# Kernel tuning notes

Hardware: AMD Instinct MI355X
Metric: run time of the kernel (lower is better)

Reference implementation:

```python
import jax, jax.numpy as jnp
import numpy as np
import math

L, B = 1024, 256
SEQ_DIM, KMER_DIM, HID = 16, 256, 64
N_LAYERS = 2
IN_DIM = SEQ_DIM + KMER_DIM + 21  # 293


def _normalize(v, eps=1e-12):
    return v / jnp.maximum(jnp.linalg.norm(v, axis=-1, keepdims=True), eps)


def _nerf_rot(a, b, c):
    # rotation matrix with columns [bc, n x bc, n] from last three backbone points
    bc = _normalize(c - b)
    n = _normalize(jnp.cross(b - a, bc))
    return jnp.stack([bc, jnp.cross(n, bc), n], axis=-1)  # (..., 3, 3)


def pnerf(c_tilde, nfrag):
    # c_tilde: (3L, B, 3) SRF coordinates; parallelized natural extension of reference frame
    Ltot, batch = c_tilde.shape[0], c_tilde.shape[1]
    k = Ltot // nfrag
    # contiguous fragments of length k, folded into the batch dim: (k, nfrag*B, 3)
    x = c_tilde.reshape(nfrag, k, batch, 3).transpose(1, 0, 2, 3).reshape(k, nfrag * batch, 3)
    init = jnp.array([[-math.sqrt(0.5), math.sqrt(1.5), 0.0],
                      [-math.sqrt(2.0), 0.0, 0.0],
                      [0.0, 0.0, 0.0]], dtype=c_tilde.dtype)
    F = nfrag * batch
    carry0 = (jnp.broadcast_to(init[0], (F, 3)),
              jnp.broadcast_to(init[1], (F, 3)),
              jnp.broadcast_to(init[2], (F, 3)))

    def extend(carry, ct):
        a, b, c = carry
        R = _nerf_rot(a, b, c)                      # (F, 3, 3)
        d = c + jnp.einsum('fij,fj->fi', R, ct)     # (F, 3)
        return (b, c, d), d

    _, frag = jax.lax.scan(extend, carry0, x)        # (k, F, 3)
    frag = frag.reshape(k, nfrag, batch, 3).transpose(1, 0, 2, 3)  # (nfrag, k, B, 3)

    # assemble fragments sequentially; init frame is identity/origin so frag 0 passes through
    carryA = (jnp.broadcast_to(init[0], (batch, 3)),
              jnp.broadcast_to(init[1], (batch, 3)),
              jnp.broadcast_to(init[2], (batch, 3)))

    def assemble(carry, fr):
        a, b, c = carry
        R = _nerf_rot(a, b, c)                      # (B, 3, 3)
        y = c + jnp.einsum('bij,kbj->kbi', R, fr)   # (k, B, 3)
        return (y[-3], y[-2], y[-1]), y

    _, ys = jax.lax.scan(assemble, carryA, frag)     # (nfrag, k, B, 3)
    return ys.reshape(nfrag * k, batch, 3)


def setup_inputs() -> dict:
    key = jax.random.key(0)
    ks = jax.random.split(key, 12)
    s = 0.05
    return {
        'seq': jax.random.randint(ks[0], (L, B), 0, 20, dtype=jnp.int64),
        'kmer': jax.random.randint(ks[1], (L, B), 0, 22 ** 3, dtype=jnp.int64),
        'pssm': jax.random.uniform(ks[2], (L, B, 21), dtype=jnp.float32),
        'length': jax.random.randint(ks[3], (L,), 1, L, dtype=jnp.int64),
        'seq_embed': jax.random.normal(ks[4], (20, SEQ_DIM), dtype=jnp.float32) * s,
        'kmer_embed': jax.random.normal(ks[5], (22 ** 3, KMER_DIM), dtype=jnp.float32) * s,
        'W0': jax.random.normal(ks[6], (IN_DIM, HID), dtype=jnp.float32) * s,
        'b0': jnp.zeros((HID,), dtype=jnp.float32),
        'We': jax.random.normal(ks[7], (HID, HID), dtype=jnp.float32) * s,
        'be': jnp.zeros((HID,), dtype=jnp.float32),
        'W1': jax.random.normal(ks[8], (HID, 9), dtype=jnp.float32) * s,
        'b1': jnp.zeros((9,), dtype=jnp.float32),
    }


def reference(seq, kmer, pssm, length, seq_embed, kmer_embed, W0, b0, We, be, W1, b1):
    s = seq_embed[seq]                                   # (L, B, 16)
    km = kmer_embed[kmer]                                # (L, B, 256)
    h = jnp.concatenate([s, km, pssm], axis=2)           # (L, B, 293)
    h = h @ W0 + b0                                      # (L, B, 64)
    # torch list-multiplication shares the SAME Linear across the n_layers blocks
    for _ in range(N_LAYERS):
        h = jax.nn.relu(h @ We + be)                     # dropout is identity at eval
    srf = h @ W1 + b1                                    # (L, B, 9)
    Ld, Bd = srf.shape[0], srf.shape[1]
    srf = srf.reshape(Ld, Bd, 3, 3).transpose(0, 2, 1, 3).reshape(3 * Ld, Bd, 3)
    return pnerf(srf, int(math.sqrt(Ld)))
```

## Files before the change

kernel.cpp:

```cpp
#include <hip/hip_runtime.h>
#include <math.h>

#define HPAD 72
#define PPAD 40

typedef short bf16x8 __attribute__((ext_vector_type(8)));
typedef float f32x4  __attribute__((ext_vector_type(4)));

__device__ __forceinline__ unsigned short f2bf(float x) {
    unsigned int u = __float_as_uint(x);
    return (unsigned short)((u + 0x7FFFu + ((u >> 16) & 1u)) >> 16);
}
__device__ __forceinline__ float bf2f(unsigned short h) {
    return __uint_as_float(((unsigned int)h) << 16);
}
__device__ __forceinline__ void split2(float x, unsigned short& h, unsigned short& l) {
    h = f2bf(x);
    l = f2bf(x - bf2f(h));
}
__device__ __forceinline__ void split2t(float x, unsigned short& h, unsigned short& l) {
    unsigned int u = __float_as_uint(x);
    h = (unsigned short)(u >> 16);
    float r = x - __uint_as_float(u & 0xFFFF0000u);
    l = f2bf(r);
}

__device__ __forceinline__ float inv_norm3(float x, float y, float z) {
    float d = fmaf(x, x, fmaf(y, y, z * z));
    return rsqrtf(fmaxf(d, 1e-24f));
}
__device__ __forceinline__ float3 f3sub(float3 a, float3 b) {
    return make_float3(a.x - b.x, a.y - b.y, a.z - b.z);
}
__device__ __forceinline__ float3 f3cross(float3 a, float3 b) {
    return make_float3(a.y * b.z - a.z * b.y,
                       a.z * b.x - a.x * b.z,
                       a.x * b.y - a.y * b.x);
}
__device__ __forceinline__ void nerf_frame(const float3& A, const float3& Bv,
                                           const float3& C, float3& bc,
                                           float3& n, float3& m3) {
    float3 w  = f3sub(C, Bv);
    float3 v  = f3sub(Bv, A);
    float3 cr = f3cross(v, w);
    float iw = inv_norm3(w.x, w.y, w.z);
    float ic = inv_norm3(cr.x, cr.y, cr.z);
    bc = make_float3(w.x * iw, w.y * iw, w.z * iw);
    n  = make_float3(cr.x * ic, cr.y * ic, cr.z * ic);
    m3 = f3cross(n, bc);
}
__device__ __forceinline__ float3 nerf_place(const float3& C, const float3& bc,
                                             const float3& m3, const float3& n,
                                             float tx, float ty, float tz) {
    return make_float3(
        fmaf(m3.x, ty, fmaf(bc.x, tx, fmaf(n.x, tz, C.x))),
        fmaf(m3.y, ty, fmaf(bc.y, tx, fmaf(n.y, tz, C.y))),
        fmaf(m3.z, ty, fmaf(bc.z, tx, fmaf(n.z, tz, C.z))));
}

__global__ __launch_bounds__(256) void tables_kernel(
    const float* __restrict__ emb, const float* __restrict__ W0,
    const float* __restrict__ se, const float* __restrict__ b0,
    const float* __restrict__ We, const float* __restrict__ W1,
    float* __restrict__ kt, float* __restrict__ seqT,
    unsigned short* __restrict__ WeTH, unsigned short* __restrict__ WeTL,
    unsigned short* __restrict__ W0pTH, unsigned short* __restrict__ W0pTL,
    unsigned short* __restrict__ W1TH, unsigned short* __restrict__ W1TL) {
    __shared__ float W0s[256][64];
    int tid = threadIdx.x;
    if (blockIdx.x < 333) {
        for (int i = tid; i < 16384; i += 256)
            W0s[i >> 6][i & 63] = W0[16 * 64 + i];
        __syncthreads();
        int j  = tid & 63;
        int wv = tid >> 6;
        int r0 = blockIdx.x * 32 + wv * 8;
        float acc[8] = {0.f,0.f,0.f,0.f,0.f,0.f,0.f,0.f};
        #pragma unroll 8
        for (int k = 0; k < 256; ++k) {
            float w = W0s[k][j];
            #pragma unroll
            for (int r = 0; r < 8; ++r) {
                int rr = r0 + r; if (rr > 10647) rr = 10647;
                acc[r] = fmaf(emb[rr * 256 + k], w, acc[r]);
            }
        }
        #pragma unroll
        for (int r = 0; r < 8; ++r)
            if (r0 + r < 10648) kt[(r0 + r) * 64 + j] = acc[r];
    } else if (blockIdx.x < 338) {
        int e = (blockIdx.x - 333) * 256 + tid;
        int r = e >> 6, j = e & 63;
        float acc = b0[j];
        #pragma unroll
        for (int k = 0; k < 16; ++k)
            acc = fmaf(se[r * 16 + k], W0[k * 64 + j], acc);
        float cs = 0.f;
        #pragma unroll
        for (int c = 0; c < 21; ++c) cs += W0[(272 + c) * 64 + j];
        seqT[r * 64 + j] = acc + 0.5f * cs;
    } else {
        #pragma unroll
        for (int i = 0; i < 16; ++i) {
            int e = i * 256 + tid;
            int k = e >> 6, n = e & 63;
            unsigned short h, l; split2(We[k * 64 + n], h, l);
            WeTH[n * 64 + k] = h; WeTL[n * 64 + k] = l;
        }
        #pragma unroll
        for (int i = 0; i < 8; ++i) {
            int e = i * 256 + tid;
            int k = e >> 6, n = e & 63;
            float w = (k < 21) ? W0[(272 + k) * 64 + n] : 0.f;
            unsigned short h, l; split2(w, h, l);
            W0pTH[n * 32 + k] = h; W0pTL[n * 32 + k] = l;
        }
        #pragma unroll
        for (int i = 0; i < 4; ++i) {
            int e = i * 256 + tid;
            int k = e >> 4, c = e & 15;
            float w = (c < 9) ? W1[k * 9 + c] : 0.f;
            unsigned short h, l; split2(w, h, l);
            W1TH[c * 64 + k] = h; W1TL[c * 64 + k] = l;
        }
    }
}

__global__ __launch_bounds__(256, 4) void mlp_kernel(
    const int* __restrict__ seq, const int* __restrict__ kmer,
    const float* __restrict__ pssm,
    const float* __restrict__ seqT, const float* __restrict__ kmerT,
    const unsigned short* __restrict__ WeTH, const unsigned short* __restrict__ WeTL,
    const unsigned short* __restrict__ W0pTH, const unsigned short* __restrict__ W0pTL,
    const unsigned short* __restrict__ W1TH, const unsigned short* __restrict__ W1TL,
    const float* __restrict__ be, const float* __restrict__ b1,
    float* __restrict__ srf_t) {

    __shared__ __align__(16) unsigned short Hah[64][HPAD];
    __shared__ __align__(16) unsigned short Hal[64][HPAD];
    __shared__ __align__(16) unsigned short ovl[2][64][HPAD];
    __shared__ int sidx[64];
    __shared__ int kidx[64];

    unsigned short (*Ph)[PPAD] = (unsigned short(*)[PPAD])(&ovl[0][0][0]);
    unsigned short (*Pl)[PPAD] = (unsigned short(*)[PPAD])(&ovl[0][0][0] + 2560);
    unsigned short (*Hbh)[HPAD] = ovl[0];
    unsigned short (*Hbl)[HPAD] = ovl[1];

    const int tid  = threadIdx.x;
    const int lane = tid & 63;
    const int wv   = __builtin_amdgcn_readfirstlane(tid >> 6);
    const int q    = lane >> 4;
    const int c16  = lane & 15;
    const int m0   = blockIdx.x * 64;
    const int n    = wv * 16 + c16;

    if (tid < 64) {
        sidx[tid] = seq[m0 + tid];
        kidx[tid] = kmer[m0 + tid];
    }
    for (int i = tid; i < 64 * 21; i += 256) {
        float v = pssm[m0 * 21 + i] - 0.5f;
        unsigned short h, l; split2t(v, h, l);
        Ph[i / 21][i % 21] = h;
        Pl[i / 21][i % 21] = l;
    }
    for (int i = tid; i < 64 * 11; i += 256) {
        Ph[i / 11][21 + (i % 11)] = 0;
        Pl[i / 11][21 + (i % 11)] = 0;
    }

    bf16x8 WeH[2], WeL[2], W1H[2], W1L[2], W0H, W0L;
    #pragma unroll
    for (int kk = 0; kk < 2; ++kk) {
        WeH[kk] = *(const bf16x8*)(WeTH + n * 64 + kk * 32 + q * 8);
        WeL[kk] = *(const bf16x8*)(WeTL + n * 64 + kk * 32 + q * 8);
        W1H[kk] = *(const bf16x8*)(W1TH + c16 * 64 + kk * 32 + q * 8);
        W1L[kk] = *(const bf16x8*)(W1TL + c16 * 64 + kk * 32 + q * 8);
    }
    W0H = *(const bf16x8*)(W0pTH + n * 32 + q * 8);
    W0L = *(const bf16x8*)(W0pTL + n * 32 + q * 8);
    const float be_n = be[n];
    const float b1h  = (c16 < 9) ? b1[c16] : 0.f;
    __syncthreads();

    f32x4 acc[4];
    #pragma unroll
    for (int t = 0; t < 4; ++t) {
        #pragma unroll
        for (int r = 0; r < 4; ++r) {
            int m = t * 16 + q * 4 + r;
            acc[t][r] = seqT[sidx[m] * 64 + n] + kmerT[kidx[m] * 64 + n];
        }
    }
    #pragma unroll
    for (int t = 0; t < 4; ++t) {
        bf16x8 ah = *(const bf16x8*)&Ph[t * 16 + c16][q * 8];
        bf16x8 al = *(const bf16x8*)&Pl[t * 16 + c16][q * 8];
        acc[t] = __builtin_amdgcn_mfma_f32_16x16x32_bf16(ah, W0H, acc[t], 0, 0, 0);
        acc[t] = __builtin_amdgcn_mfma_f32_16x16x32_bf16(al, W0H, acc[t], 0, 0, 0);
        acc[t] = __builtin_amdgcn_mfma_f32_16x16x32_bf16(ah, W0L, acc[t], 0, 0, 0);
    }
    #pragma unroll
    for (int t = 0; t < 4; ++t)
        #pragma unroll
        for (int r = 0; r < 4; ++r) {
            unsigned short h, l; split2t(acc[t][r], h, l);
            Hah[t * 16 + q * 4 + r][n] = h;
            Hal[t * 16 + q * 4 + r][n] = l;
        }
    __syncthreads();

    {
        f32x4 a1[4];
        #pragma unroll
        for (int t = 0; t < 4; ++t) {
            a1[t] = (f32x4){be_n, be_n, be_n, be_n};
            #pragma unroll
            for (int kk = 0; kk < 2; ++kk) {
                bf16x8 ah = *(const bf16x8*)&Hah[t * 16 + c16][kk * 32 + q * 8];
                bf16x8 al = *(const bf16x8*)&Hal[t * 16 + c16][kk * 32 + q * 8];
                a1[t] = __builtin_amdgcn_mfma_f32_16x16x32_bf16(ah, WeH[kk], a1[t], 0, 0, 0);
                a1[t] = __builtin_amdgcn_mfma_f32_16x16x32_bf16(al, WeH[kk], a1[t], 0, 0, 0);
                a1[t] = __builtin_amdgcn_mfma_f32_16x16x32_bf16(ah, WeL[kk], a1[t], 0, 0, 0);
            }
        }
        #pragma unroll
        for (int t = 0; t < 4; ++t)
            #pragma unroll
            for (int r = 0; r < 4; ++r) {
                unsigned short h, l; split2t(fmaxf(a1[t][r], 0.f), h, l);
                Hbh[t * 16 + q * 4 + r][n] = h;
                Hbl[t * 16 + q * 4 + r][n] = l;
            }
        __syncthreads();
    }
    {
        f32x4 a2[4];
        #pragma unroll
        for (int t = 0; t < 4; ++t) {
            a2[t] = (f32x4){be_n, be_n, be_n, be_n};
            #pragma unroll
            for (int kk = 0; kk < 2; ++kk) {
                bf16x8 ah = *(const bf16x8*)&Hbh[t * 16 + c16][kk * 32 + q * 8];
                bf16x8 al = *(const bf16x8*)&Hbl[t * 16 + c16][kk * 32 + q * 8];
                a2[t] = __builtin_amdgcn_mfma_f32_16x16x32_bf16(ah, WeH[kk], a2[t], 0, 0, 0);
                a2[t] = __builtin_amdgcn_mfma_f32_16x16x32_bf16(al, WeH[kk], a2[t], 0, 0, 0);
                a2[t] = __builtin_amdgcn_mfma_f32_16x16x32_bf16(ah, WeL[kk], a2[t], 0, 0, 0);
            }
        }
        #pragma unroll
        for (int t = 0; t < 4; ++t)
            #pragma unroll
            for (int r = 0; r < 4; ++r) {
                unsigned short h, l; split2t(fmaxf(a2[t][r], 0.f), h, l);
                Hah[t * 16 + q * 4 + r][n] = h;
                Hal[t * 16 + q * 4 + r][n] = l;
            }
        __syncthreads();
    }

    {
        f32x4 ah4 = (f32x4){b1h, b1h, b1h, b1h};
        #pragma unroll
        for (int kk = 0; kk < 2; ++kk) {
            bf16x8 ah = *(const bf16x8*)&Hah[wv * 16 + c16][kk * 32 + q * 8];
            bf16x8 al = *(const bf16x8*)&Hal[wv * 16 + c16][kk * 32 + q * 8];
            ah4 = __builtin_amdgcn_mfma_f32_16x16x32_bf16(ah, W1H[kk], ah4, 0, 0, 0);
            ah4 = __builtin_amdgcn_mfma_f32_16x16x32_bf16(al, W1H[kk], ah4, 0, 0, 0);
            ah4 = __builtin_amdgcn_mfma_f32_16x16x32_bf16(ah, W1L[kk], ah4, 0, 0, 0);
        }
        if (c16 < 9) {
            #pragma unroll
            for (int r = 0; r < 4; ++r) {
                int pos = m0 + wv * 16 + q * 4 + r;
                int l = pos >> 8, b = pos & 255;
                srf_t[(l * 9 + c16) * 256 + b] = ah4[r];
            }
        }
    }
}

__global__ __launch_bounds__(64) void extend_kernel(
    const float* __restrict__ srf_t, float* __restrict__ fragbuf,
    float* __restrict__ FPbuf) {
    int frag = blockIdx.x >> 2;
    int bb   = ((blockIdx.x & 3) << 6) + threadIdx.x;

    float3 A  = make_float3(-0.70710678118654752f, 1.22474487139158905f, 0.f);
    float3 Bv = make_float3(-1.41421356237309505f, 0.f, 0.f);
    float3 C  = make_float3(0.f, 0.f, 0.f);

    float ct0[9], ct1[9], ct2[9];
    #pragma unroll
    for (int m = 0; m < 9; ++m) {
        ct0[m] = srf_t[((frag * 32 + 0) * 9 + m) * 256 + bb];
        ct1[m] = srf_t[((frag * 32 + 1) * 9 + m) * 256 + bb];
    }

    for (int ll = 0; ll < 32; ++ll) {
        if (ll < 30) {
            #pragma unroll
            for (int m = 0; m < 9; ++m)
                ct2[m] = srf_t[((frag * 32 + ll + 2) * 9 + m) * 256 + bb];
        } else {
            #pragma unroll
            for (int m = 0; m < 9; ++m) ct2[m] = 0.f;
        }
        #pragma unroll
        for (int s3 = 0; s3 < 3; ++s3) {
            float3 bc, nn, m3;
            nerf_frame(A, Bv, C, bc, nn, m3);
            float3 d = nerf_place(C, bc, m3, nn,
                                  ct0[3 * s3 + 0], ct0[3 * s3 + 1], ct0[3 * s3 + 2]);
            int row = frag * 96 + ll * 3 + s3;
            fragbuf[(row * 3 + 0) * 256 + bb] = d.x;
            fragbuf[(row * 3 + 1) * 256 + bb] = d.y;
            fragbuf[(row * 3 + 2) * 256 + bb] = d.z;
            A = Bv; Bv = C; C = d;
        }
        #pragma unroll
        for (int m = 0; m < 9; ++m) { ct0[m] = ct1[m]; ct1[m] = ct2[m]; }
    }

    float3 bc, nn, m3;
    nerf_frame(A, Bv, C, bc, nn, m3);
    FPbuf[(frag * 12 + 0)  * 256 + bb] = bc.x;
    FPbuf[(frag * 12 + 1)  * 256 + bb] = bc.y;
    FPbuf[(frag * 12 + 2)  * 256 + bb] = bc.z;
    FPbuf[(frag * 12 + 3)  * 256 + bb] = m3.x;
    FPbuf[(frag * 12 + 4)  * 256 + bb] = m3.y;
    FPbuf[(frag * 12 + 5)  * 256 + bb] = m3.z;
    FPbuf[(frag * 12 + 6)  * 256 + bb] = nn.x;
    FPbuf[(frag * 12 + 7)  * 256 + bb] = nn.y;
    FPbuf[(frag * 12 + 8)  * 256 + bb] = nn.z;
    FPbuf[(frag * 12 + 9)  * 256 + bb] = C.x;
    FPbuf[(frag * 12 + 10) * 256 + bb] = C.y;
    FPbuf[(frag * 12 + 11) * 256 + bb] = C.z;
}

__global__ __launch_bounds__(256) void carry_kernel(
    const float* __restrict__ FPbuf, float4* __restrict__ frames) {
    __shared__ float S[384][64];
    int tid  = threadIdx.x;
    int base = blockIdx.x * 64;
    for (int i = tid; i < 384 * 64; i += 256) {
        int row = i >> 6, col = i & 63;
        S[row][col] = FPbuf[row * 256 + base + col];
    }
    __syncthreads();
    if (tid < 64) {
        int bb = base + tid;
        float3 ob = make_float3(1.f, 0.f, 0.f);
        float3 om = make_float3(0.f, 1.f, 0.f);
        float3 on = make_float3(0.f, 0.f, 1.f);
        float3 c  = make_float3(0.f, 0.f, 0.f);
        for (int f = 0; f < 32; ++f) {
            int fb = (f * 256 + bb) * 3;
            frames[fb + 0] = make_float4(ob.x, ob.y, ob.z, om.x);
            frames[fb + 1] = make_float4(om.y, om.z, on.x, on.y);
            frames[fb + 2] = make_float4(on.z, c.x, c.y, c.z);

            int r0 = f * 12;
            float3 Fb = make_float3(S[r0+0][tid], S[r0+1][tid], S[r0+2][tid]);
            float3 Fm = make_float3(S[r0+3][tid], S[r0+4][tid], S[r0+5][tid]);
            float3 Fn = make_float3(S[r0+6][tid], S[r0+7][tid], S[r0+8][tid]);
            float3 p  = make_float3(S[r0+9][tid], S[r0+10][tid], S[r0+11][tid]);

            float3 nb = make_float3(
                fmaf(ob.x,Fb.x, fmaf(om.x,Fb.y, on.x*Fb.z)),
                fmaf(ob.y,Fb.x, fmaf(om.y,Fb.y, on.y*Fb.z)),
                fmaf(ob.z,Fb.x, fmaf(om.z,Fb.y, on.z*Fb.z)));
            float3 nm = make_float3(
                fmaf(ob.x,Fm.x, fmaf(om.x,Fm.y, on.x*Fm.z)),
                fmaf(ob.y,Fm.x, fmaf(om.y,Fm.y, on.y*Fm.z)),
                fmaf(ob.z,Fm.x, fmaf(om.z,Fm.y, on.z*Fm.z)));
            float3 nn = make_float3(
                fmaf(ob.x,Fn.x, fmaf(om.x,Fn.y, on.x*Fn.z)),
                fmaf(ob.y,Fn.x, fmaf(om.y,Fn.y, on.y*Fn.z)),
                fmaf(ob.z,Fn.x, fmaf(om.z,Fn.y, on.z*Fn.z)));
            float3 nc = make_float3(
                fmaf(ob.x,p.x, fmaf(om.x,p.y, fmaf(on.x,p.z, c.x))),
                fmaf(ob.y,p.x, fmaf(om.y,p.y, fmaf(on.y,p.z, c.y))),
                fmaf(ob.z,p.x, fmaf(om.z,p.y, fmaf(on.z,p.z, c.z))));
            ob = nb; om = nm; on = nn; c = nc;
        }
    }
}

__global__ __launch_bounds__(256) void apply_kernel(
    const float* __restrict__ fragbuf, const float4* __restrict__ frames,
    float* __restrict__ out) {
    __shared__ float sm[768];
    int bb   = threadIdx.x;
    int row  = blockIdx.x;
    int frag = row / 96;

    float fx = fragbuf[(row * 3 + 0) * 256 + bb];
    float fy = fragbuf[(row * 3 + 1) * 256 + bb];
    float fz = fragbuf[(row * 3 + 2) * 256 + bb];

    int fb = (frag * 256 + bb) * 3;
    float4 f0 = frames[fb + 0];
    float4 f1 = frames[fb + 1];
    float4 f2 = frames[fb + 2];

    sm[bb * 3 + 0] = f2.y + f0.x * fx + f0.w * fy + f1.z * fz;
    sm[bb * 3 + 1] = f2.z + f0.y * fx + f1.x * fy + f1.w * fz;
    sm[bb * 3 + 2] = f2.w + f0.z * fx + f1.y * fy + f2.x * fz;
    __syncthreads();

    int base = row * 768;
    out[base + bb]       = sm[bb];
    out[base + 256 + bb] = sm[256 + bb];
    out[base + 512 + bb] = sm[512 + bb];
}

extern "C" void kernel_launch(void* const* d_in, const int* in_sizes, int n_in,
                              void* d_out, int out_size, void* d_ws, size_t ws_size,
                              hipStream_t stream) {
    const int*   seq        = (const int*)d_in[0];
    const int*   kmer       = (const int*)d_in[1];
    const float* pssm       = (const float*)d_in[2];
    const float* seq_embed  = (const float*)d_in[4];
    const float* kmer_embed = (const float*)d_in[5];
    const float* W0         = (const float*)d_in[6];
    const float* b0         = (const float*)d_in[7];
    const float* We         = (const float*)d_in[8];
    const float* be         = (const float*)d_in[9];
    const float* W1         = (const float*)d_in[10];
    const float* b1         = (const float*)d_in[11];

    float* ws      = (float*)d_ws;
    float* kmerT   = ws;
    float* seqT    = kmerT + 681472;
    float* srf_t   = seqT + 1280;
    float* fragbuf = srf_t + 2359296;
    float* frames  = fragbuf + 2359296;
    float* FPbuf   = frames + 98304;
    float* out     = (float*)d_out;

    unsigned short* WeTH  = (unsigned short*)fragbuf;
    unsigned short* WeTL  = WeTH + 4096;
    unsigned short* W0pTH = WeTL + 4096;
    unsigned short* W0pTL = W0pTH + 2048;
    unsigned short* W1TH  = W0pTL + 2048;
    unsigned short* W1TL  = W1TH + 1024;

    hipLaunchKernelGGL(tables_kernel, dim3(339), dim3(256), 0, stream,
                       kmer_embed, W0, seq_embed, b0, We, W1,
                       kmerT, seqT, WeTH, WeTL, W0pTH, W0pTL, W1TH, W1TL);
    hipLaunchKernelGGL(mlp_kernel, dim3(4096), dim3(256), 0, stream,
                       seq, kmer, pssm, seqT, kmerT,
                       WeTH, WeTL, W0pTH, W0pTL, W1TH, W1TL,
                       be, b1, srf_t);
    hipLaunchKernelGGL(extend_kernel, dim3(128), dim3(64), 0, stream,
                       srf_t, fragbuf, FPbuf);
    hipLaunchKernelGGL(carry_kernel, dim3(4), dim3(256), 0, stream,
                       FPbuf, (float4*)frames);
    hipLaunchKernelGGL(apply_kernel, dim3(3072), dim3(256), 0, stream,
                       fragbuf, (float4*)frames, out);
}
```

Measured before the change: 202.3 us.

## Use split-bf16 MFMA for kmer table, register-load pssm in MLP, deepen extend prefetch

```diff
diff --git a/kernel.cpp b/kernel.cpp
--- a/kernel.cpp
+++ b/kernel.cpp
@@ -2,7 +2,6 @@
 #include <math.h>
 
 #define HPAD 72
-#define PPAD 40
 
 typedef short bf16x8 __attribute__((ext_vector_type(8)));
 typedef float f32x4  __attribute__((ext_vector_type(4)));
@@ -66,30 +65,62 @@
     unsigned short* __restrict__ WeTH, unsigned short* __restrict__ WeTL,
     unsigned short* __restrict__ W0pTH, unsigned short* __restrict__ W0pTL,
     unsigned short* __restrict__ W1TH, unsigned short* __restrict__ W1TL) {
-    __shared__ float W0s[256][64];
     int tid = threadIdx.x;
-    if (blockIdx.x < 333) {
-        for (int i = tid; i < 16384; i += 256)
-            W0s[i >> 6][i & 63] = W0[16 * 64 + i];
-        __syncthreads();
-        int j  = tid & 63;
-        int wv = tid >> 6;
-        int r0 = blockIdx.x * 32 + wv * 8;
-        float acc[8] = {0.f,0.f,0.f,0.f,0.f,0.f,0.f,0.f};
-        #pragma unroll 8
-        for (int k = 0; k < 256; ++k) {
-            float w = W0s[k][j];
-            #pragma unroll
-            for (int r = 0; r < 8; ++r) {
-                int rr = r0 + r; if (rr > 10647) rr = 10647;
-                acc[r] = fmaf(emb[rr * 256 + k], w, acc[r]);
-            }
-        }
-        #pragma unroll
-        for (int r = 0; r < 8; ++r)
-            if (r0 + r < 10648) kt[(r0 + r) * 64 + j] = acc[r];
-    } else if (blockIdx.x < 338) {
-        int e = (blockIdx.x - 333) * 256 + tid;
+    if (blockIdx.x < 167) {
+        const int lane = tid & 63;
+        const int wv   = __builtin_amdgcn_readfirstlane(tid >> 6);
+        const int q    = lane >> 4;
+        const int c16  = lane & 15;
+        const int r0   = blockIdx.x * 64;
+        const int n    = wv * 16 + c16;
+
+        bf16x8 BH[8], BL[8];
+        #pragma unroll
+        for (int kt8 = 0; kt8 < 8; ++kt8)
+            #pragma unroll
+            for (int j = 0; j < 8; ++j) {
+                float w = W0[(16 + kt8 * 32 + q * 8 + j) * 64 + n];
+                unsigned short h, l; split2t(w, h, l);
+                BH[kt8][j] = (short)h; BL[kt8][j] = (short)l;
+            }
+
+        f32x4 acc[4];
+        #pragma unroll
+        for (int t = 0; t < 4; ++t) acc[t] = (f32x4){0.f, 0.f, 0.f, 0.f};
+
+        #pragma unroll
+        for (int kt8 = 0; kt8 < 8; ++kt8) {
+            #pragma unroll
+            for (int t = 0; t < 4; ++t) {
+                int rr = r0 + t * 16 + c16;
+                if (rr > 10647) rr = 10647;
+                const float* ap = emb + rr * 256 + kt8 * 32 + q * 8;
+                float4 a0 = *(const float4*)ap;
+                float4 a1 = *(const float4*)(ap + 4);
+                bf16x8 ah, al;
+                unsigned short h, l;
+                split2t(a0.x, h, l); ah[0] = (short)h; al[0] = (short)l;
+                split2t(a0.y, h, l); ah[1] = (short)h; al[1] = (short)l;
+                split2t(a0.z, h, l); ah[2] = (short)h; al[2] = (short)l;
+                split2t(a0.w, h, l); ah[3] = (short)h; al[3] = (short)l;
+                split2t(a1.x, h, l); ah[4] = (short)h; al[4] = (short)l;
+                split2t(a1.y, h, l); ah[5] = (short)h; al[5] = (short)l;
+                split2t(a1.z, h, l); ah[6] = (short)h; al[6] = (short)l;
+                split2t(a1.w, h, l); ah[7] = (short)h; al[7] = (short)l;
+                acc[t] = __builtin_amdgcn_mfma_f32_16x16x32_bf16(ah, BH[kt8], acc[t], 0, 0, 0);
+                acc[t] = __builtin_amdgcn_mfma_f32_16x16x32_bf16(al, BH[kt8], acc[t], 0, 0, 0);
+                acc[t] = __builtin_amdgcn_mfma_f32_16x16x32_bf16(ah, BL[kt8], acc[t], 0, 0, 0);
+            }
+        }
+        #pragma unroll
+        for (int t = 0; t < 4; ++t)
+            #pragma unroll
+            for (int r = 0; r < 4; ++r) {
+                int row = r0 + t * 16 + q * 4 + r;
+                if (row < 10648) kt[row * 64 + n] = acc[t][r];
+            }
+    } else if (blockIdx.x < 172) {
+        int e = (blockIdx.x - 167) * 256 + tid;
         int r = e >> 6, j = e & 63;
         float acc = b0[j];
         #pragma unroll
@@ -138,14 +169,8 @@
 
     __shared__ __align__(16) unsigned short Hah[64][HPAD];
     __shared__ __align__(16) unsigned short Hal[64][HPAD];
-    __shared__ __align__(16) unsigned short ovl[2][64][HPAD];
-    __shared__ int sidx[64];
-    __shared__ int kidx[64];
-
-    unsigned short (*Ph)[PPAD] = (unsigned short(*)[PPAD])(&ovl[0][0][0]);
-    unsigned short (*Pl)[PPAD] = (unsigned short(*)[PPAD])(&ovl[0][0][0] + 2560);
-    unsigned short (*Hbh)[HPAD] = ovl[0];
-    unsigned short (*Hbl)[HPAD] = ovl[1];
+    __shared__ __align__(16) unsigned short Hbh[64][HPAD];
+    __shared__ __align__(16) unsigned short Hbl[64][HPAD];
 
     const int tid  = threadIdx.x;
     const int lane = tid & 63;
@@ -155,19 +180,29 @@
     const int m0   = blockIdx.x * 64;
     const int n    = wv * 16 + c16;
 
-    if (tid < 64) {
-        sidx[tid] = seq[m0 + tid];
-        kidx[tid] = kmer[m0 + tid];
-    }
-    for (int i = tid; i < 64 * 21; i += 256) {
-        float v = pssm[m0 * 21 + i] - 0.5f;
-        unsigned short h, l; split2t(v, h, l);
-        Ph[i / 21][i % 21] = h;
-        Pl[i / 21][i % 21] = l;
-    }
-    for (int i = tid; i < 64 * 11; i += 256) {
-        Ph[i / 11][21 + (i % 11)] = 0;
-        Pl[i / 11][21 + (i % 11)] = 0;
+    f32x4 acc[4];
+    #pragma unroll
+    for (int t = 0; t < 4; ++t) {
+        #pragma unroll
+        for (int r = 0; r < 4; ++r) {
+            int m  = t * 16 + q * 4 + r;
+            int s  = seq[m0 + m];
+            int km = kmer[m0 + m];
+            acc[t][r] = seqT[s * 64 + n] + kmerT[km * 64 + n];
+        }
+    }
+
+    bf16x8 PAH[4], PAL[4];
+    #pragma unroll
+    for (int t = 0; t < 4; ++t) {
+        int m = m0 + t * 16 + c16;
+        #pragma unroll
+        for (int j = 0; j < 8; ++j) {
+            int k = q * 8 + j;
+            float v = (k < 21) ? (pssm[m * 21 + k] - 0.5f) : 0.f;
+            unsigned short h, l; split2t(v, h, l);
+            PAH[t][j] = (short)h; PAL[t][j] = (short)l;
+        }
     }
 
     bf16x8 WeH[2], WeL[2], W1H[2], W1L[2], W0H, W0L;
@@ -182,24 +217,12 @@
     W0L = *(const bf16x8*)(W0pTL + n * 32 + q * 8);
     const float be_n = be[n];
     const float b1h  = (c16 < 9) ? b1[c16] : 0.f;
-    __syncthreads();
-
-    f32x4 acc[4];
+
     #pragma unroll
     for (int t = 0; t < 4; ++t) {
-        #pragma unroll
-        for (int r = 0; r < 4; ++r) {
-            int m = t * 16 + q * 4 + r;
-            acc[t][r] = seqT[sidx[m] * 64 + n] + kmerT[kidx[m] * 64 + n];
-        }
-    }
-    #pragma unroll
-    for (int t = 0; t < 4; ++t) {
-        bf16x8 ah = *(const bf16x8*)&Ph[t * 16 + c16][q * 8];
-        bf16x8 al = *(const bf16x8*)&Pl[t * 16 + c16][q * 8];
-        acc[t] = __builtin_amdgcn_mfma_f32_16x16x32_bf16(ah, W0H, acc[t], 0, 0, 0);
-        acc[t] = __builtin_amdgcn_mfma_f32_16x16x32_bf16(al, W0H, acc[t], 0, 0, 0);
-        acc[t] = __builtin_amdgcn_mfma_f32_16x16x32_bf16(ah, W0L, acc[t], 0, 0, 0);
+        acc[t] = __builtin_amdgcn_mfma_f32_16x16x32_bf16(PAH[t], W0H, acc[t], 0, 0, 0);
+        acc[t] = __builtin_amdgcn_mfma_f32_16x16x32_bf16(PAL[t], W0H, acc[t], 0, 0, 0);
+        acc[t] = __builtin_amdgcn_mfma_f32_16x16x32_bf16(PAH[t], W0L, acc[t], 0, 0, 0);
     }
     #pragma unroll
     for (int t = 0; t < 4; ++t)
@@ -291,21 +314,22 @@
     float3 Bv = make_float3(-1.41421356237309505f, 0.f, 0.f);
     float3 C  = make_float3(0.f, 0.f, 0.f);
 
-    float ct0[9], ct1[9], ct2[9];
+    float ct0[9], ct1[9], ct2[9], ct3[9];
     #pragma unroll
     for (int m = 0; m < 9; ++m) {
         ct0[m] = srf_t[((frag * 32 + 0) * 9 + m) * 256 + bb];
         ct1[m] = srf_t[((frag * 32 + 1) * 9 + m) * 256 + bb];
+        ct2[m] = srf_t[((frag * 32 + 2) * 9 + m) * 256 + bb];
     }
 
     for (int ll = 0; ll < 32; ++ll) {
-        if (ll < 30) {
+        if (ll < 29) {
             #pragma unroll
             for (int m = 0; m < 9; ++m)
-                ct2[m] = srf_t[((frag * 32 + ll + 2) * 9 + m) * 256 + bb];
+                ct3[m] = srf_t[((frag * 32 + ll + 3) * 9 + m) * 256 + bb];
         } else {
             #pragma unroll
-            for (int m = 0; m < 9; ++m) ct2[m] = 0.f;
+            for (int m = 0; m < 9; ++m) ct3[m] = 0.f;
         }
         #pragma unroll
         for (int s3 = 0; s3 < 3; ++s3) {
@@ -320,7 +344,7 @@
             A = Bv; Bv = C; C = d;
         }
         #pragma unroll
-        for (int m = 0; m < 9; ++m) { ct0[m] = ct1[m]; ct1[m] = ct2[m]; }
+        for (int m = 0; m < 9; ++m) { ct0[m] = ct1[m]; ct1[m] = ct2[m]; ct2[m] = ct3[m]; }
     }
 
     float3 bc, nn, m3;
@@ -447,7 +471,7 @@
     unsigned short* W1TH  = W0pTL + 2048;
     unsigned short* W1TL  = W1TH + 1024;
 
-    hipLaunchKernelGGL(tables_kernel, dim3(339), dim3(256), 0, stream,
+    hipLaunchKernelGGL(tables_kernel, dim3(173), dim3(256), 0, stream,
                        kmer_embed, W0, seq_embed, b0, We, W1,
                        kmerT, seqT, WeTH, WeTL, W0pTH, W0pTL, W1TH, W1TL);
     hipLaunchKernelGGL(mlp_kernel, dim3(4096), dim3(256), 0, stream,
```

Result: faster. 196.9 us (-2.7%).
